# Kernel optimization log

Hardware: AMD Instinct MI355X
Metric: run time of the kernel (lower is better)

The kernel has to match this reference:

```python
import jax, jax.numpy as jnp
import numpy as np


def _lstm_layer(x, W_ih, W_hh, b_ih, b_hh, reverse=False):
    """Single LSTM layer. x: [T, B, D] -> outputs [T, B, H]. PyTorch gate order i,f,g,o."""
    H = W_hh.shape[-1]
    B = x.shape[1]
    # precompute input contribution for all steps
    xg = jnp.einsum('tbd,gd->tbg', x, W_ih) + b_ih + b_hh  # [T, B, 4H]

    def step(carry, xt):
        h, c = carry
        gates = xt + h @ W_hh.T
        i, f, g, o = jnp.split(gates, 4, axis=-1)
        c = jax.nn.sigmoid(f) * c + jax.nn.sigmoid(i) * jnp.tanh(g)
        h = jax.nn.sigmoid(o) * jnp.tanh(c)
        return (h, c), h

    init = (jnp.zeros((B, H), x.dtype), jnp.zeros((B, H), x.dtype))
    _, hs = jax.lax.scan(step, init, xg, reverse=reverse)
    return hs


def setup_inputs() -> dict:
    key = jax.random.key(0)
    ks = jax.random.split(key, 24)
    B, S, L = 64, 256, 16
    VOCAB, CVOCAB, NCLS = 50000, 128, 50
    E, CE, H = 100, 50, 300
    IN0 = E + CE          # 150, bilstm layer-0 input
    IN1 = 2 * H           # 600, bilstm layer-1 input

    def u(k, shape, fan):
        lim = 1.0 / np.sqrt(fan)
        return jax.random.uniform(k, shape, jnp.float32, -lim, lim)

    inp = {
        'word_ids': jax.random.randint(ks[0], (B, S), 0, VOCAB, jnp.int32),
        'char_ids': jax.random.randint(ks[1], (B, S, L), 0, CVOCAB, jnp.int32),
        'word_embed': jax.random.normal(ks[2], (VOCAB, E), jnp.float32) * 0.1,
        'char_embed': jax.random.normal(ks[3], (CVOCAB, CE), jnp.float32) * 0.1,
        # char LSTM: 2 layers, unidirectional, input==hidden==CE -> stack over layers
        'cWih': u(ks[4], (2, 4 * CE, CE), CE),
        'cWhh': u(ks[5], (2, 4 * CE, CE), CE),
        'cbih': u(ks[6], (2, 4 * CE), CE),
        'cbhh': u(ks[7], (2, 4 * CE), CE),
        # bilstm layer 0: stack over directions [2, ...]
        'b0_Wih': u(ks[8], (2, 4 * H, IN0), H),
        'b0_Whh': u(ks[9], (2, 4 * H, H), H),
        'b0_bih': u(ks[10], (2, 4 * H), H),
        'b0_bhh': u(ks[11], (2, 4 * H), H),
        # bilstm layer 1
        'b1_Wih': u(ks[12], (2, 4 * H, IN1), H),
        'b1_Whh': u(ks[13], (2, 4 * H, H), H),
        'b1_bih': u(ks[14], (2, 4 * H), H),
        'b1_bhh': u(ks[15], (2, 4 * H), H),
        'fcW': u(ks[16], (NCLS, 2 * H), 2 * H),
        'fcb': u(ks[17], (NCLS,), 2 * H),
    }
    return inp


def reference(word_ids, char_ids, word_embed, char_embed, cWih, cWhh, cbih, cbhh,
              b0_Wih, b0_Whh, b0_bih, b0_bhh, b1_Wih, b1_Whh, b1_bih, b1_bhh,
              fcW, fcb):
    B, S, L = char_ids.shape
    CE = char_embed.shape[1]

    # --- char-level path: batch all B*S words through the 2-layer char LSTM ---
    ch = char_embed[char_ids.reshape(B * S, L)]            # [BS, L, CE]
    x = jnp.transpose(ch, (1, 0, 2))                       # [L, BS, CE]
    x = _lstm_layer(x, cWih[0], cWhh[0], cbih[0], cbhh[0])
    x = _lstm_layer(x, cWih[1], cWhh[1], cbih[1], cbhh[1])
    char_feat = x[-1].reshape(B, S, CE)                    # last step of top layer

    # --- word path + concat ---
    emb = word_embed[word_ids]                             # [B, S, E]
    seq = jnp.transpose(jnp.concatenate([emb, char_feat], axis=-1), (1, 0, 2))  # [S, B, 150]

    # --- 2-layer bidirectional LSTM ---
    f0 = _lstm_layer(seq, b0_Wih[0], b0_Whh[0], b0_bih[0], b0_bhh[0])
    r0 = _lstm_layer(seq, b0_Wih[1], b0_Whh[1], b0_bih[1], b0_bhh[1], reverse=True)
    h0 = jnp.concatenate([f0, r0], axis=-1)                # [S, B, 600]
    f1 = _lstm_layer(h0, b1_Wih[0], b1_Whh[0], b1_bih[0], b1_bhh[0])
    r1 = _lstm_layer(h0, b1_Wih[1], b1_Whh[1], b1_bih[1], b1_bhh[1], reverse=True)
    h1 = jnp.concatenate([f1, r1], axis=-1)                # [S, B, 600]

    out = jnp.einsum('sbh,ch->bsc', h1, fcW) + fcb         # [B, S, NCLS]
    return jax.nn.log_softmax(out, axis=-1)
```

## Files before the change

kernel.cpp:

```cpp
#include <hip/hip_runtime.h>

typedef unsigned short u16;
typedef unsigned int   u32;
typedef unsigned long long u64;
typedef __attribute__((ext_vector_type(8))) short bf16x8;
typedef __attribute__((ext_vector_type(4))) float f32x4;

#define MFMA16(a,b,c) __builtin_amdgcn_mfma_f32_16x16x32_bf16((a),(b),(c),0,0,0)

#define NWG   19
#define HP    320
#define GP    304
#define XGB   4096
#define SLOTS 257

static const size_t OFF_XG  = 0;
static const size_t SZ_XG   = (size_t)2*256*NWG*XGB*2;
static const size_t OFF_H0  = OFF_XG + SZ_XG;
static const size_t SZ_HB   = (size_t)2*SLOTS*64*HP*2;
static const size_t OFF_H1  = OFF_H0 + SZ_HB;
static const size_t OFF_CF  = OFF_H1 + SZ_HB;
static const size_t SZ_CF   = (size_t)16384*64*2;
static const size_t OFF_W0  = OFF_CF + SZ_CF;
static const size_t SZ_W0   = (size_t)2432*160*2;
static const size_t OFF_W1  = OFF_W0 + SZ_W0;
static const size_t SZ_W1   = (size_t)2432*640*2;
static const size_t OFF_WFC = OFF_W1 + SZ_W1;
static const size_t SZ_WFC  = (size_t)64*640*2;
static const size_t OFF_B0  = OFF_WFC + SZ_WFC;
static const size_t OFF_B1  = OFF_B0 + 2432*4;
static const size_t OFF_BFC = OFF_B1 + 2432*4;
static const size_t OFF_DT  = OFF_BFC + 64*4;
static const size_t WS_NEED = OFF_DT + 4;

__device__ __forceinline__ float bf2f(u16 u){ union{u32 i; float f;} v; v.i=(u32)u<<16; return v.f; }
__device__ __forceinline__ u16 f2bf(float f){ union{float f; u32 u;} v; v.f=f; u32 r=v.u+0x7fffu+((v.u>>16)&1u); return (u16)(r>>16); }
__device__ __forceinline__ float sigf(float x){ return __builtin_amdgcn_rcpf(1.f+__builtin_amdgcn_exp2f(-1.4426950408889634f*x)); }
__device__ __forceinline__ float tanhf_(float x){ return 2.f*__builtin_amdgcn_rcpf(1.f+__builtin_amdgcn_exp2f(-2.8853900817779268f*x))-1.f; }
__device__ __forceinline__ float ldf(const void* p, size_t i, bool f32){
  return f32 ? ((const float*)p)[i] : bf2f(((const u16*)p)[i]);
}
__device__ __forceinline__ u16 ldh(const void* p, size_t i, bool f32){
  return f32 ? f2bf(((const float*)p)[i]) : ((const u16*)p)[i];
}

__global__ __launch_bounds__(256,1) void k_detect(const u16* __restrict__ probe, u32* __restrict__ cnt)
{
  int c = 0;
  for (int i = threadIdx.x; i < 65536; i += 256) {
    u16 v = probe[i];
    if (((v >> 7) & 0xFF) == 0xFF) ++c;
  }
  if (c) atomicAdd(cnt, (u32)c);
}

__global__ __launch_bounds__(256,4) void k_prep(
    const void* __restrict__ b0_Wih, const void* __restrict__ b0_bih, const void* __restrict__ b0_bhh,
    const void* __restrict__ b1_Wih, const void* __restrict__ b1_bih, const void* __restrict__ b1_bhh,
    const void* __restrict__ fcW,    const void* __restrict__ fcb,
    u16* __restrict__ W0p, u16* __restrict__ W1p, u16* __restrict__ Wfc,
    float* __restrict__ bias0, float* __restrict__ bias1, float* __restrict__ biasfc,
    const u32* __restrict__ dtf)
{
  const bool isf32 = (*dtf >= 8u);
  const int T0 = 2432*160, T1 = 2432*640, T2 = 64*640;
  const int total = T0 + T1 + T2 + 2432 + 2432 + 64;
  for (int i = blockIdx.x*256 + threadIdx.x; i < total; i += gridDim.x*256) {
    int x = i;
    if (x < T0) {
      int n = x/160, k = x%160;
      int dir = n/1216, cc = n%1216, g = cc/GP, uu = cc%GP;
      W0p[x] = (uu<300 && k<150) ? ldh(b0_Wih, ((size_t)dir*1200 + g*300 + uu)*150 + k, isf32) : (u16)0;
      continue;
    }
    x -= T0;
    if (x < T1) {
      int n = x/640, k = x%640;
      int dir = n/1216, cc = n%1216, g = cc/GP, uu = cc%GP;
      int part = (k>=320), ui = k - part*320;
      W1p[x] = (uu<300 && ui<300) ? ldh(b1_Wih, ((size_t)dir*1200 + g*300 + uu)*600 + part*300 + ui, isf32) : (u16)0;
      continue;
    }
    x -= T1;
    if (x < T2) {
      int n = x/640, k = x%640;
      int part = (k>=320), ui = k - part*320;
      Wfc[x] = (n<50 && ui<300) ? ldh(fcW, (size_t)n*600 + part*300 + ui, isf32) : (u16)0;
      continue;
    }
    x -= T2;
    if (x < 2432) {
      int dir = x/1216, cc = x%1216, g = cc/GP, uu = cc%GP;
      bias0[x] = (uu<300) ? ldf(b0_bih, dir*1200+g*300+uu, isf32) + ldf(b0_bhh, dir*1200+g*300+uu, isf32) : 0.f;
      continue;
    }
    x -= 2432;
    if (x < 2432) {
      int dir = x/1216, cc = x%1216, g = cc/GP, uu = cc%GP;
      bias1[x] = (uu<300) ? ldf(b1_bih, dir*1200+g*300+uu, isf32) + ldf(b1_bhh, dir*1200+g*300+uu, isf32) : 0.f;
      continue;
    }
    x -= 2432;
    biasfc[x] = (x<50) ? ldf(fcb, x, isf32) : 0.f;
  }
}

__global__ __launch_bounds__(256,1) void k_char(
    const int* __restrict__ char_ids, const void* __restrict__ cemb,
    const void* __restrict__ cWih, const void* __restrict__ cWhh,
    const void* __restrict__ cbih, const void* __restrict__ cbhh,
    u16* __restrict__ charfeat, const u32* __restrict__ dtf)
{
  __shared__ u16 emb[128][64];
  __shared__ int ids[16][64];
  __shared__ u16 h0s[64][64];
  __shared__ u16 h1s[64][64];
  const bool isf32 = (*dtf >= 8u);
  const int tid = threadIdx.x;
  const int g0  = blockIdx.x * 64;

  for (int e = tid; e < 128*64; e += 256) {
    int row = e>>6, col = e&63;
    (&emb[0][0])[e] = (col<50) ? ldh(cemb, row*50 + col, isf32) : (u16)0;
  }
  for (int e = tid; e < 1024; e += 256) ids[e&15][e>>4] = char_ids[(size_t)g0*16 + e];
  for (int e = tid; e < 4096; e += 256) { (&h0s[0][0])[e] = 0; (&h1s[0][0])[e] = 0; }
  __syncthreads();

  const int w = tid>>6, lane = tid&63, quad = lane>>4, lcol = lane&15;
  const int u = w*16 + lcol;

  bf16x8 Wf[2][4][4];
  #pragma unroll
  for (int l=0; l<2; ++l)
    #pragma unroll
    for (int g=0; g<4; ++g)
      #pragma unroll
      for (int kt=0; kt<4; ++kt) {
        union { bf16x8 v; u16 h[8]; } t8;
        #pragma unroll
        for (int q=0; q<8; ++q) {
          int k = kt*32 + quad*8 + q;
          u16 val = 0;
          if (u < 50) {
            if (k < 50)                  val = ldh(cWih, l*10000 + (g*50+u)*50 + k, isf32);
            else if (k >= 64 && k < 114) val = ldh(cWhh, l*10000 + (g*50+u)*50 + (k-64), isf32);
          }
          t8.h[q] = val;
        }
        Wf[l][g][kt] = t8.v;
      }
  float bs[2][4];
  #pragma unroll
  for (int l=0; l<2; ++l)
    #pragma unroll
    for (int g=0; g<4; ++g)
      bs[l][g] = (u<50) ? ldf(cbih, l*200+g*50+u, isf32) + ldf(cbhh, l*200+g*50+u, isf32) : 0.f;

  float c0[4][4] = {}; float c1[4][4] = {};
  float h0n[4][4], h1n[4][4];

  for (int t=0; t<16; ++t) {
    #pragma unroll
    for (int m=0; m<4; ++m) {
      f32x4 acc[4];
      #pragma unroll
      for (int g=0; g<4; ++g) acc[g] = (f32x4){bs[0][g], bs[0][g], bs[0][g], bs[0][g]};
      #pragma unroll
      for (int kt=0; kt<4; ++kt) {
        bf16x8 a;
        if (kt < 2) { int id = ids[t][m*16+lcol]; a = *(const bf16x8*)&emb[id][kt*32 + quad*8]; }
        else        { a = *(const bf16x8*)&h0s[m*16+lcol][(kt-2)*32 + quad*8]; }
        #pragma unroll
        for (int g=0; g<4; ++g) acc[g] = MFMA16(a, Wf[0][g][kt], acc[g]);
      }
      #pragma unroll
      for (int r=0; r<4; ++r) {
        float cn = sigf(acc[1][r])*c0[m][r] + sigf(acc[0][r])*tanhf_(acc[2][r]);
        c0[m][r] = cn;
        h0n[m][r] = sigf(acc[3][r]) * tanhf_(cn);
      }
    }
    __syncthreads();
    #pragma unroll
    for (int m=0; m<4; ++m)
      #pragma unroll
      for (int r=0; r<4; ++r) h0s[m*16 + quad*4 + r][u] = f2bf(h0n[m][r]);
    __syncthreads();
    #pragma unroll
    for (int m=0; m<4; ++m) {
      f32x4 acc[4];
      #pragma unroll
      for (int g=0; g<4; ++g) acc[g] = (f32x4){bs[1][g], bs[1][g], bs[1][g], bs[1][g]};
      #pragma unroll
      for (int kt=0; kt<4; ++kt) {
        bf16x8 a = (kt<2) ? *(const bf16x8*)&h0s[m*16+lcol][kt*32 + quad*8]
                          : *(const bf16x8*)&h1s[m*16+lcol][(kt-2)*32 + quad*8];
        #pragma unroll
        for (int g=0; g<4; ++g) acc[g] = MFMA16(a, Wf[1][g][kt], acc[g]);
      }
      #pragma unroll
      for (int r=0; r<4; ++r) {
        float cn = sigf(acc[1][r])*c1[m][r] + sigf(acc[0][r])*tanhf_(acc[2][r]);
        c1[m][r] = cn;
        h1n[m][r] = sigf(acc[3][r]) * tanhf_(cn);
      }
    }
    __syncthreads();
    #pragma unroll
    for (int m=0; m<4; ++m)
      #pragma unroll
      for (int r=0; r<4; ++r) h1s[m*16 + quad*4 + r][u] = f2bf(h1n[m][r]);
    __syncthreads();
  }
  for (int e = tid; e < 4096; e += 256)
    charfeat[(size_t)(g0 + (e>>6))*64 + (e&63)] = (&h1s[0][0])[e];
}

__device__ __forceinline__ size_t xg_addr(int n, int row){
  int dir = n/1216, cc = n%1216, g = cc/GP, cg = cc%GP, jj = cg>>4, uc = cg&15;
  int t = row>>6, b = row&63;
  return (((size_t)dir*256 + t)*NWG + jj)*XGB + (g*16 + uc)*64 + b;
}

__global__ __launch_bounds__(256,2) void k_proj0(
    const int* __restrict__ word_ids, const void* __restrict__ wemb,
    const u16* __restrict__ charfeat, const u16* __restrict__ W0p,
    const float* __restrict__ bias0, u16* __restrict__ xg, const u32* __restrict__ dtf)
{
  __shared__ u16 As[64][160];
  __shared__ u16 Bst[64][160];
  const bool isf32 = (*dtf >= 8u);
  const int tid = threadIdx.x;
  const int r0 = blockIdx.x*64, n0 = blockIdx.y*64;
  u32* Asu = (u32*)&As[0][0];
  u32* Bsu = (u32*)&Bst[0][0];
  for (int e = tid; e < 64*80; e += 256) {
    int rr = e/80, cu = e%80;
    int r = r0 + rr, t = r>>6, b = r&63;
    u32 v;
    if (cu < 50) {
      int wid = word_ids[b*256 + t];
      if (isf32) {
        const float* wf = (const float*)wemb;
        v = (u32)f2bf(wf[(size_t)wid*100 + cu*2]) | ((u32)f2bf(wf[(size_t)wid*100 + cu*2 + 1]) << 16);
      } else {
        v = ((const u32*)wemb)[(size_t)wid*50 + cu];
      }
    }
    else if (cu < 75) { v = ((const u32*)charfeat)[(size_t)r*32 + (cu-50)]; }
    else              v = 0;
    Asu[rr*80 + cu] = v;
  }
  for (int e = tid; e < 64*80; e += 256) {
    int n = e/80, cu = e%80;
    Bsu[n*80 + cu] = ((const u32*)W0p)[(size_t)(n0+n)*80 + cu];
  }
  __syncthreads();
  const int w = tid>>6, lane = tid&63, quad = lane>>4, lcol = lane&15;
  f32x4 acc[4] = {};
  #pragma unroll
  for (int kt=0; kt<5; ++kt) {
    bf16x8 a = *(const bf16x8*)&As[w*16+lcol][kt*32 + quad*8];
    #pragma unroll
    for (int nt=0; nt<4; ++nt) {
      bf16x8 bb = *(const bf16x8*)&Bst[nt*16+lcol][kt*32 + quad*8];
      acc[nt] = MFMA16(a, bb, acc[nt]);
    }
  }
  #pragma unroll
  for (int nt=0; nt<4; ++nt) {
    int n = n0 + nt*16 + lcol;
    float bia = bias0[n];
    #pragma unroll
    for (int r=0; r<4; ++r) {
      int row = r0 + w*16 + quad*4 + r;
      xg[xg_addr(n, row)] = f2bf(acc[nt][r] + bia);
    }
  }
}

__global__ __launch_bounds__(256,2) void k_proj1(
    const u16* __restrict__ Hbuf, const u16* __restrict__ W1p,
    const float* __restrict__ bias1, u16* __restrict__ xg)
{
  __shared__ u16 As[64][128];
  __shared__ u16 Bst[64][128];
  const int tid = threadIdx.x;
  const int r0 = blockIdx.x*64, n0 = blockIdx.y*64;
  const u32* Hu = (const u32*)Hbuf;
  const u32* Wu = (const u32*)W1p;
  u32* Asu = (u32*)&As[0][0];
  u32* Bsu = (u32*)&Bst[0][0];
  const int w = tid>>6, lane = tid&63, quad = lane>>4, lcol = lane&15;
  f32x4 acc[4] = {};
  for (int ch=0; ch<5; ++ch) {
    __syncthreads();
    for (int e = tid; e < 4096; e += 256) {
      int rr = e>>6, cu = e&63;
      int r = r0 + rr, t = r>>6, b = r&63;
      int kk = ch*128 + cu*2;
      int part = (kk>=320), off = kk - part*320;
      Asu[e] = Hu[(((size_t)part*SLOTS + (part ? 256-t : t+1))*64 + b)*160 + (off>>1)];
    }
    for (int e = tid; e < 4096; e += 256) {
      int n = e>>6, cu = e&63;
      Bsu[e] = Wu[(size_t)(n0+n)*320 + ch*64 + cu];
    }
    __syncthreads();
    #pragma unroll
    for (int kt=0; kt<4; ++kt) {
      bf16x8 a = *(const bf16x8*)&As[w*16+lcol][kt*32 + quad*8];
      #pragma unroll
      for (int nt=0; nt<4; ++nt) {
        bf16x8 bb = *(const bf16x8*)&Bst[nt*16+lcol][kt*32 + quad*8];
        acc[nt] = MFMA16(a, bb, acc[nt]);
      }
    }
  }
  #pragma unroll
  for (int nt=0; nt<4; ++nt) {
    int n = n0 + nt*16 + lcol;
    float bia = bias1[n];
    #pragma unroll
    for (int r=0; r<4; ++r) {
      int row = r0 + w*16 + quad*4 + r;
      xg[xg_addr(n, row)] = f2bf(acc[nt][r] + bia);
    }
  }
}

__global__ __launch_bounds__(256,1) void k_scan(
    const u16* __restrict__ xg, const void* __restrict__ Whh,
    u16* __restrict__ Hbuf, const u32* __restrict__ dtf)
{
  const bool isf32 = (*dtf >= 8u);
  const int bx = blockIdx.x;
  const int d = bx / NWG, j = bx % NWG;
  const int tid = threadIdx.x;
  const int w = tid>>6, lane = tid&63, quad = lane>>4, lcol = lane&15;
  const int u = j*16 + lcol;
  const int brow = w*16;

  bf16x8 Bf[4][10];
  #pragma unroll
  for (int g=0; g<4; ++g)
    #pragma unroll
    for (int kt=0; kt<10; ++kt) {
      union { bf16x8 v; u16 h[8]; } t8;
      #pragma unroll
      for (int q=0; q<8; ++q) {
        int k = kt*32 + quad*8 + q;
        t8.h[q] = (u < 300 && k < 300) ? ldh(Whh, ((size_t)d*1200 + g*300 + u)*300 + k, isf32) : (u16)0;
      }
      Bf[g][kt] = t8.v;
    }

  float c[4] = {0.f,0.f,0.f,0.f};

  for (int t=0; t<256; ++t) {
    const int tt = d ? (255 - t) : t;
    const volatile u64* xp = (const volatile u64*)(xg + (((size_t)d*256 + tt)*NWG + j)*XGB);
    u64 xq[4];
    #pragma unroll
    for (int g=0; g<4; ++g)
      xq[g] = xp[((g*16 + lcol)*64 + brow + quad*4) >> 2];

    union HU { bf16x8 v; u64 q[2]; u32 w4[4]; };
    HU a[10];
    const u16* hp = Hbuf + (((size_t)d*SLOTS + t)*64 + (brow + lcol))*HP + quad*8;
    while (true) {
      #pragma unroll
      for (int kt=0; kt<10; ++kt) {
        a[kt].q[0] = __hip_atomic_load((const u64*)(hp + kt*32),     __ATOMIC_RELAXED, __HIP_MEMORY_SCOPE_AGENT);
        a[kt].q[1] = __hip_atomic_load((const u64*)(hp + kt*32 + 4), __ATOMIC_RELAXED, __HIP_MEMORY_SCOPE_AGENT);
      }
      u32 mx = 0u;
      #pragma unroll
      for (int kt=0; kt<10; ++kt)
        #pragma unroll
        for (int i=0; i<4; ++i) { u32 ww = a[kt].w4[i]; mx = (ww > mx) ? ww : mx; }
      if (__ballot(mx != 0xFFFFFFFFu) == ~0ull) break;
      __builtin_amdgcn_s_sleep(1);
    }

    f32x4 acc[4];
    #pragma unroll
    for (int g=0; g<4; ++g) {
      union { u64 q; u16 h[4]; } t4; t4.q = xq[g];
      #pragma unroll
      for (int r=0; r<4; ++r) acc[g][r] = bf2f(t4.h[r]);
    }
    #pragma unroll
    for (int kt=0; kt<10; ++kt) {
      #pragma unroll
      for (int g=0; g<4; ++g) acc[g] = MFMA16(a[kt].v, Bf[g][kt], acc[g]);
    }
    #pragma unroll
    for (int r=0; r<4; ++r) {
      float cn = sigf(acc[1][r])*c[r] + sigf(acc[0][r])*tanhf_(acc[2][r]);
      c[r] = cn;
      float h = sigf(acc[3][r]) * tanhf_(cn);
      u32 mine = (u32)f2bf(h);
      u32 other = (u32)__shfl_xor((int)mine, 1, 64);
      if ((lcol & 1) == 0) {
        u32 word = mine | (other << 16);
        int b = brow + quad*4 + r;
        size_t e = (((size_t)d*SLOTS + (t+1))*64 + b)*HP + j*16 + lcol;
        __hip_atomic_store((u32*)(Hbuf + e), word, __ATOMIC_RELAXED, __HIP_MEMORY_SCOPE_AGENT);
      }
    }
    if (j == NWG-1) {
      #pragma unroll
      for (int r=0; r<4; ++r) {
        if ((lcol & 1) == 0) {
          int b = brow + quad*4 + r;
          size_t e2 = (((size_t)d*SLOTS + (t+1))*64 + b)*HP + 304 + lcol;
          __hip_atomic_store((u32*)(Hbuf + e2), 0u, __ATOMIC_RELAXED, __HIP_MEMORY_SCOPE_AGENT);
        }
      }
    }
  }
}

__global__ __launch_bounds__(256,2) void k_fc(
    const u16* __restrict__ Hbuf, const u16* __restrict__ Wfc,
    const float* __restrict__ biasfc, void* __restrict__ outv, const u32* __restrict__ dtf)
{
  __shared__ u16 As[64][128];
  __shared__ u16 Bst[64][128];
  const bool isf32 = (*dtf >= 8u);
  const int tid = threadIdx.x;
  const int r0 = blockIdx.x*64;
  const u32* Hu = (const u32*)Hbuf;
  const u32* Wu = (const u32*)Wfc;
  u32* Asu = (u32*)&As[0][0];
  u32* Bsu = (u32*)&Bst[0][0];
  const int w = tid>>6, lane = tid&63, quad = lane>>4, lcol = lane&15;
  f32x4 acc[4] = {};
  for (int ch=0; ch<5; ++ch) {
    __syncthreads();
    for (int e = tid; e < 4096; e += 256) {
      int rr = e>>6, cu = e&63;
      int r = r0 + rr, t = r>>6, b = r&63;
      int kk = ch*128 + cu*2;
      int part = (kk>=320), off = kk - part*320;
      Asu[e] = Hu[(((size_t)part*SLOTS + (part ? 256-t : t+1))*64 + b)*160 + (off>>1)];
    }
    for (int e = tid; e < 4096; e += 256) {
      int n = e>>6, cu = e&63;
      Bsu[e] = Wu[(size_t)n*320 + ch*64 + cu];
    }
    __syncthreads();
    #pragma unroll
    for (int kt=0; kt<4; ++kt) {
      bf16x8 a = *(const bf16x8*)&As[w*16+lcol][kt*32 + quad*8];
      #pragma unroll
      for (int nt=0; nt<4; ++nt) {
        bf16x8 bb = *(const bf16x8*)&Bst[nt*16+lcol][kt*32 + quad*8];
        acc[nt] = MFMA16(a, bb, acc[nt]);
      }
    }
  }
  float vals[4][4];
  #pragma unroll
  for (int nt=0; nt<4; ++nt) {
    int cc = nt*16 + lcol;
    float bia = biasfc[cc];
    #pragma unroll
    for (int r=0; r<4; ++r) vals[nt][r] = (cc < 50) ? (acc[nt][r] + bia) : -3.0e38f;
  }
  float lz[4];
  #pragma unroll
  for (int r=0; r<4; ++r) {
    float m = fmaxf(fmaxf(vals[0][r], vals[1][r]), fmaxf(vals[2][r], vals[3][r]));
    #pragma unroll
    for (int dd=1; dd<16; dd<<=1) m = fmaxf(m, __shfl_xor(m, dd, 64));
    float s = 0.f;
    #pragma unroll
    for (int nt=0; nt<4; ++nt) s += __builtin_amdgcn_exp2f((vals[nt][r]-m)*1.4426950408889634f);
    #pragma unroll
    for (int dd=1; dd<16; dd<<=1) s += __shfl_xor(s, dd, 64);
    lz[r] = m + __builtin_amdgcn_logf(s)*0.6931471805599453f;
  }
  #pragma unroll
  for (int nt=0; nt<4; ++nt) {
    int cc = nt*16 + lcol;
    if (cc < 50) {
      #pragma unroll
      for (int r=0; r<4; ++r) {
        int row = r0 + w*16 + quad*4 + r;
        int t = row>>6, b = row&63;
        size_t idx = ((size_t)b*256 + t)*50 + cc;
        float v = vals[nt][r] - lz[r];
        if (isf32) ((float*)outv)[idx] = v;
        else       ((u16*)outv)[idx] = f2bf(v);
      }
    }
  }
}

extern "C" void kernel_launch(void* const* d_in, const int* in_sizes, int n_in,
                              void* d_out, int out_size, void* d_ws, size_t ws_size,
                              hipStream_t stream) {
  (void)in_sizes; (void)n_in; (void)out_size;
  if (ws_size < WS_NEED) return;

  const int* word_ids = (const int*)d_in[0];
  const int* char_ids = (const int*)d_in[1];
  const void* wemb   = d_in[2];
  const void* cemb   = d_in[3];
  const void* cWih   = d_in[4];
  const void* cWhh   = d_in[5];
  const void* cbih   = d_in[6];
  const void* cbhh   = d_in[7];
  const void* b0_Wih = d_in[8];
  const void* b0_Whh = d_in[9];
  const void* b0_bih = d_in[10];
  const void* b0_bhh = d_in[11];
  const void* b1_Wih = d_in[12];
  const void* b1_Whh = d_in[13];
  const void* b1_bih = d_in[14];
  const void* b1_bhh = d_in[15];
  const void* fcW    = d_in[16];
  const void* fcb    = d_in[17];

  char* ws = (char*)d_ws;
  u16*   xg   = (u16*)(ws + OFF_XG);
  u16*   H0   = (u16*)(ws + OFF_H0);
  u16*   H1   = (u16*)(ws + OFF_H1);
  u16*   cf   = (u16*)(ws + OFF_CF);
  u16*   W0p  = (u16*)(ws + OFF_W0);
  u16*   W1p  = (u16*)(ws + OFF_W1);
  u16*   Wfc  = (u16*)(ws + OFF_WFC);
  float* bia0 = (float*)(ws + OFF_B0);
  float* bia1 = (float*)(ws + OFF_B1);
  float* biaf = (float*)(ws + OFF_BFC);
  u32*   dtf  = (u32*)(ws + OFF_DT);

  hipMemsetAsync(H0, 0xFF, SZ_HB, stream);
  hipMemsetAsync(H1, 0xFF, SZ_HB, stream);
  hipMemsetAsync(H0,                       0, (size_t)64*HP*2, stream);
  hipMemsetAsync(H0 + (size_t)SLOTS*64*HP, 0, (size_t)64*HP*2, stream);
  hipMemsetAsync(H1,                       0, (size_t)64*HP*2, stream);
  hipMemsetAsync(H1 + (size_t)SLOTS*64*HP, 0, (size_t)64*HP*2, stream);
  hipMemsetAsync(dtf, 0, 4, stream);

  k_detect<<<1, 256, 0, stream>>>((const u16*)wemb, dtf);
  k_prep<<<7780, 256, 0, stream>>>(b0_Wih, b0_bih, b0_bhh, b1_Wih, b1_bih, b1_bhh,
                                   fcW, fcb, W0p, W1p, Wfc, bia0, bia1, biaf, dtf);
  k_char<<<256, 256, 0, stream>>>(char_ids, cemb, cWih, cWhh, cbih, cbhh, cf, dtf);
  k_proj0<<<dim3(256,38), 256, 0, stream>>>(word_ids, wemb, cf, W0p, bia0, xg, dtf);
  k_scan<<<2*NWG, 256, 0, stream>>>(xg, b0_Whh, H0, dtf);
  k_proj1<<<dim3(256,38), 256, 0, stream>>>(H0, W1p, bia1, xg);
  k_scan<<<2*NWG, 256, 0, stream>>>(xg, b1_Whh, H1, dtf);
  k_fc<<<256, 256, 0, stream>>>(H1, Wfc, biaf, d_out, dtf);
}
```

Baseline: 2.910 ms.

## Retile scan hidden-state and xg buffers for coalesced per-step loads

Changes the hidden-state buffer layout to k-tile-major blocks of 32 units by 64 batch rows, so each wave's per-step polling loads are contiguous. The xg layout is permuted so each lane reads one contiguous u64, and the volatile qualifier is dropped. The padded-column zero stores are removed and the last k-tile load is masked, and the char kernel's shared arrays are padded against bank conflicts. The consumers (proj1, fc) are updated to the new indexing, which adds address arithmetic and a branch there.

```diff
diff --git a/kernel.cpp b/kernel.cpp
--- a/kernel.cpp
+++ b/kernel.cpp
@@ -13,11 +13,12 @@
 #define GP    304
 #define XGB   4096
 #define SLOTS 257
+#define HSLOT 20480
 
 static const size_t OFF_XG  = 0;
 static const size_t SZ_XG   = (size_t)2*256*NWG*XGB*2;
 static const size_t OFF_H0  = OFF_XG + SZ_XG;
-static const size_t SZ_HB   = (size_t)2*SLOTS*64*HP*2;
+static const size_t SZ_HB   = (size_t)2*SLOTS*HSLOT*2;
 static const size_t OFF_H1  = OFF_H0 + SZ_HB;
 static const size_t OFF_CF  = OFF_H1 + SZ_HB;
 static const size_t SZ_CF   = (size_t)16384*64*2;
@@ -113,8 +114,8 @@
 {
   __shared__ u16 emb[128][64];
   __shared__ int ids[16][64];
-  __shared__ u16 h0s[64][64];
-  __shared__ u16 h1s[64][64];
+  __shared__ u16 h0s[64][72];
+  __shared__ u16 h1s[64][72];
   const bool isf32 = (*dtf >= 8u);
   const int tid = threadIdx.x;
   const int g0  = blockIdx.x * 64;
@@ -124,7 +125,7 @@
     (&emb[0][0])[e] = (col<50) ? ldh(cemb, row*50 + col, isf32) : (u16)0;
   }
   for (int e = tid; e < 1024; e += 256) ids[e&15][e>>4] = char_ids[(size_t)g0*16 + e];
-  for (int e = tid; e < 4096; e += 256) { (&h0s[0][0])[e] = 0; (&h1s[0][0])[e] = 0; }
+  for (int e = tid; e < 4096; e += 256) { h0s[e>>6][e&63] = 0; h1s[e>>6][e&63] = 0; }
   __syncthreads();
 
   const int w = tid>>6, lane = tid&63, quad = lane>>4, lcol = lane&15;
@@ -214,13 +215,14 @@
     __syncthreads();
   }
   for (int e = tid; e < 4096; e += 256)
-    charfeat[(size_t)(g0 + (e>>6))*64 + (e&63)] = (&h1s[0][0])[e];
+    charfeat[(size_t)(g0 + (e>>6))*64 + (e&63)] = h1s[e>>6][e&63];
 }
 
 __device__ __forceinline__ size_t xg_addr(int n, int row){
   int dir = n/1216, cc = n%1216, g = cc/GP, cg = cc%GP, jj = cg>>4, uc = cg&15;
   int t = row>>6, b = row&63;
-  return (((size_t)dir*256 + t)*NWG + jj)*XGB + (g*16 + uc)*64 + b;
+  size_t off = ((size_t)(g*4 + (b>>4))*64 + ((b>>2)&3)*16 + uc)*4 + (b&3);
+  return (((size_t)dir*256 + t)*NWG + jj)*XGB + off;
 }
 
 __global__ __launch_bounds__(256,2) void k_proj0(
@@ -300,8 +302,13 @@
       int rr = e>>6, cu = e&63;
       int r = r0 + rr, t = r>>6, b = r&63;
       int kk = ch*128 + cu*2;
-      int part = (kk>=320), off = kk - part*320;
-      Asu[e] = Hu[(((size_t)part*SLOTS + (part ? 256-t : t+1))*64 + b)*160 + (off>>1)];
+      int part = (kk>=320), uu = kk - part*320;
+      u32 v = 0;
+      if (uu < 304) {
+        size_t slot = part ? (size_t)(256 - t) : (size_t)(t + 1);
+        v = Hu[(size_t)part*SLOTS*10240 + slot*10240 + ((size_t)(uu>>5)*64 + b)*16 + ((uu&31)>>1)];
+      }
+      Asu[e] = v;
     }
     for (int e = tid; e < 4096; e += 256) {
       int n = e>>6, cu = e&63;
@@ -341,6 +348,7 @@
   const int w = tid>>6, lane = tid&63, quad = lane>>4, lcol = lane&15;
   const int u = j*16 + lcol;
   const int brow = w*16;
+  const int ktj = j>>1, kub = (j&1)*16;
 
   bf16x8 Bf[4][10];
   #pragma unroll
@@ -357,24 +365,30 @@
     }
 
   float c[4] = {0.f,0.f,0.f,0.f};
+  const bool okq = (quad < 2);
 
   for (int t=0; t<256; ++t) {
     const int tt = d ? (255 - t) : t;
-    const volatile u64* xp = (const volatile u64*)(xg + (((size_t)d*256 + tt)*NWG + j)*XGB);
+    const u64* xp = (const u64*)(xg + (((size_t)d*256 + tt)*NWG + j)*XGB);
     u64 xq[4];
     #pragma unroll
-    for (int g=0; g<4; ++g)
-      xq[g] = xp[((g*16 + lcol)*64 + brow + quad*4) >> 2];
+    for (int g=0; g<4; ++g) xq[g] = xp[(g*4 + w)*64 + lane];
 
     union HU { bf16x8 v; u64 q[2]; u32 w4[4]; };
     HU a[10];
-    const u16* hp = Hbuf + (((size_t)d*SLOTS + t)*64 + (brow + lcol))*HP + quad*8;
+    const u64* hp = (const u64*)Hbuf + (((size_t)d*SLOTS + t)*HSLOT >> 2);
     while (true) {
       #pragma unroll
-      for (int kt=0; kt<10; ++kt) {
-        a[kt].q[0] = __hip_atomic_load((const u64*)(hp + kt*32),     __ATOMIC_RELAXED, __HIP_MEMORY_SCOPE_AGENT);
-        a[kt].q[1] = __hip_atomic_load((const u64*)(hp + kt*32 + 4), __ATOMIC_RELAXED, __HIP_MEMORY_SCOPE_AGENT);
-      }
+      for (int kt=0; kt<9; ++kt) {
+        size_t bi = (size_t)(kt*64 + brow + lcol)*8 + quad*2;
+        a[kt].q[0] = __hip_atomic_load(hp + bi,     __ATOMIC_RELAXED, __HIP_MEMORY_SCOPE_AGENT);
+        a[kt].q[1] = __hip_atomic_load(hp + bi + 1, __ATOMIC_RELAXED, __HIP_MEMORY_SCOPE_AGENT);
+      }
+      if (okq) {
+        size_t bi = (size_t)(9*64 + brow + lcol)*8 + quad*2;
+        a[9].q[0] = __hip_atomic_load(hp + bi,     __ATOMIC_RELAXED, __HIP_MEMORY_SCOPE_AGENT);
+        a[9].q[1] = __hip_atomic_load(hp + bi + 1, __ATOMIC_RELAXED, __HIP_MEMORY_SCOPE_AGENT);
+      } else { a[9].q[0] = 0; a[9].q[1] = 0; }
       u32 mx = 0u;
       #pragma unroll
       for (int kt=0; kt<10; ++kt)
@@ -396,6 +410,7 @@
       #pragma unroll
       for (int g=0; g<4; ++g) acc[g] = MFMA16(a[kt].v, Bf[g][kt], acc[g]);
     }
+    size_t sbase = ((size_t)d*SLOTS + (t+1))*HSLOT;
     #pragma unroll
     for (int r=0; r<4; ++r) {
       float cn = sigf(acc[1][r])*c[r] + sigf(acc[0][r])*tanhf_(acc[2][r]);
@@ -406,18 +421,8 @@
       if ((lcol & 1) == 0) {
         u32 word = mine | (other << 16);
         int b = brow + quad*4 + r;
-        size_t e = (((size_t)d*SLOTS + (t+1))*64 + b)*HP + j*16 + lcol;
+        size_t e = sbase + (size_t)(ktj*64 + b)*32 + kub + lcol;
         __hip_atomic_store((u32*)(Hbuf + e), word, __ATOMIC_RELAXED, __HIP_MEMORY_SCOPE_AGENT);
-      }
-    }
-    if (j == NWG-1) {
-      #pragma unroll
-      for (int r=0; r<4; ++r) {
-        if ((lcol & 1) == 0) {
-          int b = brow + quad*4 + r;
-          size_t e2 = (((size_t)d*SLOTS + (t+1))*64 + b)*HP + 304 + lcol;
-          __hip_atomic_store((u32*)(Hbuf + e2), 0u, __ATOMIC_RELAXED, __HIP_MEMORY_SCOPE_AGENT);
-        }
       }
     }
   }
@@ -444,8 +449,13 @@
       int rr = e>>6, cu = e&63;
       int r = r0 + rr, t = r>>6, b = r&63;
       int kk = ch*128 + cu*2;
-      int part = (kk>=320), off = kk - part*320;
-      Asu[e] = Hu[(((size_t)part*SLOTS + (part ? 256-t : t+1))*64 + b)*160 + (off>>1)];
+      int part = (kk>=320), uu = kk - part*320;
+      u32 v = 0;
+      if (uu < 304) {
+        size_t slot = part ? (size_t)(256 - t) : (size_t)(t + 1);
+        v = Hu[(size_t)part*SLOTS*10240 + slot*10240 + ((size_t)(uu>>5)*64 + b)*16 + ((uu&31)>>1)];
+      }
+      Asu[e] = v;
     }
     for (int e = tid; e < 4096; e += 256) {
       int n = e>>6, cu = e&63;
@@ -540,10 +550,10 @@
 
   hipMemsetAsync(H0, 0xFF, SZ_HB, stream);
   hipMemsetAsync(H1, 0xFF, SZ_HB, stream);
-  hipMemsetAsync(H0,                       0, (size_t)64*HP*2, stream);
-  hipMemsetAsync(H0 + (size_t)SLOTS*64*HP, 0, (size_t)64*HP*2, stream);
-  hipMemsetAsync(H1,                       0, (size_t)64*HP*2, stream);
-  hipMemsetAsync(H1 + (size_t)SLOTS*64*HP, 0, (size_t)64*HP*2, stream);
+  hipMemsetAsync(H0,                      0, (size_t)HSLOT*2, stream);
+  hipMemsetAsync(H0 + (size_t)SLOTS*HSLOT, 0, (size_t)HSLOT*2, stream);
+  hipMemsetAsync(H1,                      0, (size_t)HSLOT*2, stream);
+  hipMemsetAsync(H1 + (size_t)SLOTS*HSLOT, 0, (size_t)HSLOT*2, stream);
   hipMemsetAsync(dtf, 0, 4, stream);
 
   k_detect<<<1, 256, 0, stream>>>((const u16*)wemb, dtf);
```

Measured after the change: 2.612 ms. 1.11x faster.
